# Optimization experiments

Measured on AMD Instinct MI355X. Metric: run time of the kernel, lower is better.

## Reference

```python
import jax, jax.numpy as jnp
import numpy as np

N_NODES = 100000


def _gcn_layer(x, W, b, src, dst, n):
    # PyG GCNConv: x' = D^-1/2 (A+I) D^-1/2 (x W) + b, with self-loops added.
    x = x @ W  # [N, out]
    loop = jnp.arange(n, dtype=src.dtype)
    src_f = jnp.concatenate([src, loop])
    dst_f = jnp.concatenate([dst, loop])
    deg = jax.ops.segment_sum(jnp.ones_like(dst_f, dtype=x.dtype), dst_f, num_segments=n)
    dinv = jnp.where(deg > 0, jax.lax.rsqrt(deg), 0.0)
    norm = dinv[src_f] * dinv[dst_f]  # [E+N]
    msgs = x[src_f] * norm[:, None]   # gather + scale
    out = jax.ops.segment_sum(msgs, dst_f, num_segments=n)
    return out + b


def setup_inputs() -> dict:
    key = jax.random.key(0)
    ks = jax.random.split(key, 16)
    inputFeatures = jax.random.normal(ks[0], (N_NODES, 64), dtype=jnp.float32)
    edge_index = jax.random.randint(ks[1], (2, 1000000), 0, N_NODES, dtype=jnp.int64)

    def lin(k, fan_in, fan_out):
        s = 1.0 / np.sqrt(fan_in)
        return jax.random.uniform(k, (fan_in, fan_out), jnp.float32, -s, s)

    return {
        "inputFeatures": inputFeatures,
        "W1": lin(ks[2], 64, 100), "b1": jnp.zeros((100,), jnp.float32),
        "W2": lin(ks[3], 100, 50), "b2": jnp.zeros((50,), jnp.float32),
        "W3": lin(ks[4], 50, 25), "b3": jnp.zeros((25,), jnp.float32),
        "Wl1": lin(ks[5], 25, 25), "bl1": jnp.zeros((25,), jnp.float32),
        "Wl2": lin(ks[6], 25, 10), "bl2": jnp.zeros((10,), jnp.float32),
        "Wl3": lin(ks[7], 10, 1), "bl3": jnp.zeros((1,), jnp.float32),
        "edge_index": edge_index,
    }


def reference(inputFeatures, W1, b1, W2, b2, W3, b3, Wl1, bl1, Wl2, bl2, Wl3, bl3, edge_index):
    src, dst = edge_index[0], edge_index[1]
    n = inputFeatures.shape[0]
    x = jax.nn.relu(_gcn_layer(inputFeatures, W1, b1, src, dst, n))
    x = jax.nn.relu(_gcn_layer(x, W2, b2, src, dst, n))
    x = jax.nn.relu(_gcn_layer(x, W3, b3, src, dst, n))
    x = jax.nn.relu(x @ Wl1 + bl1)
    x = jax.nn.relu(x @ Wl2 + bl2)
    x = jax.nn.relu(x @ Wl3 + bl3)
    return x  # [N, 1]
```

## Files before the change

kernel.cpp:

```cpp
#include <hip/hip_runtime.h>
#include <hip/hip_fp16.h>
#include <cstdint>

constexpr int BSHIFT = 9;
constexpr int NBUCK  = 256;
constexpr int BUCKET_CAP = 6144;
constexpr int BN = 1 << BSHIFT;

struct alignas(16) H8 { __half2 a, b, c, d; };
struct alignas(8)  H4 { __half2 a, b; };

typedef _Float16 f16x8 __attribute__((ext_vector_type(8)));
typedef float    f32x4 __attribute__((ext_vector_type(4)));

__device__ __forceinline__ float4 add4(float4 a, float4 b) {
    return make_float4(a.x + b.x, a.y + b.y, a.z + b.z, a.w + b.w);
}
__device__ __forceinline__ float4 mul4s(float4 a, float s) {
    return make_float4(a.x * s, a.y * s, a.z * s, a.w * s);
}
__device__ __forceinline__ void acc_h8(float4& A0, float4& A1, const H8 v, float s) {
    float2 f0 = __half22float2(v.a), f1 = __half22float2(v.b);
    float2 f2 = __half22float2(v.c), f3 = __half22float2(v.d);
    A0.x = fmaf(f0.x, s, A0.x); A0.y = fmaf(f0.y, s, A0.y);
    A0.z = fmaf(f1.x, s, A0.z); A0.w = fmaf(f1.y, s, A0.w);
    A1.x = fmaf(f2.x, s, A1.x); A1.y = fmaf(f2.y, s, A1.y);
    A1.z = fmaf(f3.x, s, A1.z); A1.w = fmaf(f3.y, s, A1.w);
}


constexpr int EPT = 16;
__global__ __launch_bounds__(256) void partition_pack(
    const int* __restrict__ src, const int* __restrict__ dst,
    int* __restrict__ bucketCur, int* __restrict__ pairs, int ne, int nEdgeBlocks,
    const float* __restrict__ W1, const float* __restrict__ W2,
    const float* __restrict__ W3,
    __half* __restrict__ P1, __half* __restrict__ P2, __half* __restrict__ P3) {
    if (blockIdx.x == (unsigned)nEdgeBlocks) {
        int t = threadIdx.x;
        for (int i = t; i < 7 * 2 * 64 * 8; i += 256) {
            int j = i & 7, lane = (i >> 3) & 63, f = i >> 9;
            int mt = f >> 1, kf = f & 1;
            int k = kf * 32 + (lane >> 4) * 8 + j;
            int m = mt * 16 + (lane & 15);
            P1[i] = __float2half_rn(m < 100 ? W1[k * 100 + m] : 0.0f);
        }
        for (int i = t; i < 4 * 4 * 64 * 8; i += 256) {
            int j = i & 7, lane = (i >> 3) & 63, f = i >> 9;
            int mt = f >> 2, kf = f & 3;
            int k = kf * 32 + (lane >> 4) * 8 + j;
            int m = mt * 16 + (lane & 15);
            P2[i] = __float2half_rn((k < 100 && m < 50) ? W2[k * 50 + m] : 0.0f);
        }
        for (int i = t; i < 2 * 2 * 64 * 8; i += 256) {
            int j = i & 7, lane = (i >> 3) & 63, f = i >> 9;
            int mt = f >> 1, kf = f & 1;
            int k = kf * 32 + (lane >> 4) * 8 + j;
            int m = mt * 16 + (lane & 15);
            P3[i] = __float2half_rn((k < 50 && m < 25) ? W3[k * 25 + m] : 0.0f);
        }
        return;
    }
    __shared__ int lcnt[NBUCK];
    __shared__ int lbase[NBUCK];
    int base = blockIdx.x * (256 * EPT);
    if (threadIdx.x < NBUCK) lcnt[threadIdx.x] = 0;
    __syncthreads();
    int2 ed[EPT];
    int  rnk[EPT];
#pragma unroll
    for (int j = 0; j < EPT; ++j) {
        int e = base + j * 256 + threadIdx.x;
        if (e < ne) {
            int d = dst[e];
            ed[j] = make_int2(src[e], d);
            rnk[j] = atomicAdd(&lcnt[d >> BSHIFT], 1);
        } else {
            ed[j].y = -1;
        }
    }
    __syncthreads();
    if (threadIdx.x < NBUCK) {
        int c = lcnt[threadIdx.x];
        lbase[threadIdx.x] = c ? atomicAdd(&bucketCur[threadIdx.x], c) : 0;
    }
    __syncthreads();
#pragma unroll
    for (int j = 0; j < EPT; ++j) {
        if (ed[j].y >= 0) {
            int b = ed[j].y >> BSHIFT;
            int p = lbase[b] + rnk[j];
            if (p < BUCKET_CAP)
                pairs[(size_t)b * BUCKET_CAP + p] =
                    (ed[j].x << BSHIFT) | (ed[j].y & (BN - 1));
        }
    }
}

__global__ __launch_bounds__(256) void bucket_csr_scan(
    const int* __restrict__ pairs, const int* __restrict__ bucketCnt,
    int* __restrict__ offs, float* __restrict__ dinv, int* __restrict__ csr,
    int n, int ne, int nbuckets) {
    __shared__ int hist[BN];
    __shared__ int cur[BN];
    __shared__ int tmp[256];
    __shared__ int baseS;
    int b = blockIdx.x;
    int t = threadIdx.x;

    int c = (t < (unsigned)nbuckets) ? bucketCnt[t] : 0;
    tmp[t] = c;
    __syncthreads();
    for (int off = 1; off < 256; off <<= 1) {
        int v = (t >= (unsigned)off) ? tmp[t - off] : 0;
        __syncthreads();
        tmp[t] += v;
        __syncthreads();
    }
    if (t == 0) {
        baseS = b ? tmp[b - 1] : 0;
        if (b == 0) offs[n] = ne;
    }
    __syncthreads();
    int base = baseS;
    int cnt  = bucketCnt[b];
    const int* pb = pairs + (size_t)b * BUCKET_CAP;
    int nodeLo = b << BSHIFT;

    hist[t] = 0;
    hist[t + 256] = 0;
    __syncthreads();
    for (int e = t; e < cnt; e += 256)
        atomicAdd(&hist[pb[e] & (BN - 1)], 1);
    __syncthreads();

    int l0 = 2 * t, l1 = l0 + 1;
    int h0 = hist[l0], h1 = hist[l1];
    tmp[t] = h0 + h1;
    __syncthreads();
    for (int off = 1; off < 256; off <<= 1) {
        int v = (t >= (unsigned)off) ? tmp[t - off] : 0;
        __syncthreads();
        tmp[t] += v;
        __syncthreads();
    }
    int e0 = tmp[t] - (h0 + h1);
    int e1 = e0 + h0;
    int g0 = nodeLo + l0, g1 = nodeLo + l1;
    if (g0 < n) { offs[g0] = base + e0; dinv[g0] = rsqrtf((float)(h0 + 1)); }
    if (g1 < n) { offs[g1] = base + e1; dinv[g1] = rsqrtf((float)(h1 + 1)); }
    cur[l0] = e0;
    cur[l1] = e1;
    __syncthreads();

    for (int e = t; e < cnt; e += 256) {
        int p = pb[e];
        int pos = atomicAdd(&cur[p & (BN - 1)], 1);
        csr[base + pos] = ((unsigned)p) >> BSHIFT;
    }
}

__global__ void cvt_scale_f32_f16(const float* __restrict__ x, const float* __restrict__ dinv,
                                  __half* __restrict__ o, int n4) {
    int i = blockIdx.x * blockDim.x + threadIdx.x;
    if (i < n4) {
        float dv = dinv[i >> 4];
        float4 v = ((const float4*)x)[i];
        H4 h;
        h.a = __floats2half2_rn(v.x * dv, v.y * dv);
        h.b = __floats2half2_rn(v.z * dv, v.w * dv);
        ((H4*)o)[i] = h;
    }
}

constexpr int XSP = 72;
constexpr int HPS = 136;
__global__ __launch_bounds__(256, 4) void agg1gemm12(
    const __half* __restrict__ x, const int* __restrict__ offs,
    const int* __restrict__ csr, const float* __restrict__ dinv,
    const __half* __restrict__ P1, const float* __restrict__ b1,
    const __half* __restrict__ P2, __half* __restrict__ out, int n) {
    __shared__ alignas(16) _Float16 Xs[64 * XSP];
    __shared__ alignas(16) _Float16 Hs[64 * HPS];
    int tid = threadIdx.x, lane = tid & 63, w = tid >> 6;
    int lg = lane >> 4, lr = lane & 15;
    int blockBase = blockIdx.x * 64;

    for (int i = tid; i < 64 * 2; i += 256) {
        f16x8 zz = {};
        *(f16x8*)&Hs[(i >> 1) * HPS + 112 + (i & 1) * 8] = zz;
    }

    int f0 = (lane & 7) * 8;
#pragma unroll
    for (int p = 0; p < 2; ++p) {
        int nl = w * 16 + p * 8 + (lane >> 3);
        int node = blockBase + nl;
        float4 z4 = make_float4(0.f, 0.f, 0.f, 0.f);
        float4 a00 = z4, a01 = z4, a10 = z4, a11 = z4, a20 = z4, a21 = z4, a30 = z4, a31 = z4;
        float dv = 0.0f;
        if (node < n) {
            dv = dinv[node];
            H8 sv = *(const H8*)&x[(size_t)node * 64 + f0];
            acc_h8(a00, a01, sv, 1.0f);
            int e0 = offs[node], e1 = offs[node + 1];
            int e = e0;
            for (; e + 4 <= e1; e += 4) {
                int i0 = csr[e], i1 = csr[e + 1], i2 = csr[e + 2], i3 = csr[e + 3];
                H8 v0 = *(const H8*)&x[(size_t)i0 * 64 + f0];
                H8 v1 = *(const H8*)&x[(size_t)i1 * 64 + f0];
                H8 v2 = *(const H8*)&x[(size_t)i2 * 64 + f0];
                H8 v3 = *(const H8*)&x[(size_t)i3 * 64 + f0];
                acc_h8(a00, a01, v0, 1.0f);
                acc_h8(a10, a11, v1, 1.0f);
                acc_h8(a20, a21, v2, 1.0f);
                acc_h8(a30, a31, v3, 1.0f);
            }
            for (; e < e1; ++e) {
                H8 v = *(const H8*)&x[(size_t)csr[e] * 64 + f0];
                acc_h8(a00, a01, v, 1.0f);
            }
        }
        float4 A0 = add4(add4(a00, a10), add4(a20, a30));
        float4 A1 = add4(add4(a01, a11), add4(a21, a31));
        A0 = mul4s(A0, dv);
        A1 = mul4s(A1, dv);
        H8 h;
        h.a = __floats2half2_rn(A0.x, A0.y);
        h.b = __floats2half2_rn(A0.z, A0.w);
        h.c = __floats2half2_rn(A1.x, A1.y);
        h.d = __floats2half2_rn(A1.z, A1.w);
        *(H8*)&Xs[nl * XSP + f0] = h;
    }
    __syncthreads();

    const f16x8* P1v = (const f16x8*)P1;
    float b1v[7];
#pragma unroll
    for (int mt = 0; mt < 7; ++mt) {
        int m = mt * 16 + lr;
        b1v[mt] = (m < 100) ? b1[m] : 0.0f;
    }
    {
        int rowL = w * 16 + lr;
        f16x8 a0 = *(const f16x8*)&Xs[rowL * XSP + lg * 8];
        f16x8 a1 = *(const f16x8*)&Xs[rowL * XSP + 32 + lg * 8];
        int hbase = w * 16;
#pragma unroll
        for (int mt = 0; mt < 7; ++mt) {
            f16x8 w0 = P1v[(mt * 2 + 0) * 64 + lane];
            f16x8 w1 = P1v[(mt * 2 + 1) * 64 + lane];
            f32x4 acc = {};
            acc = __builtin_amdgcn_mfma_f32_16x16x32_f16(a0, w0, acc, 0, 0, 0);
            acc = __builtin_amdgcn_mfma_f32_16x16x32_f16(a1, w1, acc, 0, 0, 0);
            int col = mt * 16 + lr;
#pragma unroll
            for (int i = 0; i < 4; ++i) {
                int rloc = hbase + lg * 4 + i;
                Hs[rloc * HPS + col] = (_Float16)fmaxf(acc[i] + b1v[mt], 0.0f);
            }
        }
    }
    __syncthreads();

    const f16x8* P2v = (const f16x8*)P2;
    int lbase = w * 16;
    const _Float16* hrow = &Hs[(size_t)(lbase + lr) * HPS];
    f16x8 a0 = *(const f16x8*)&hrow[lg * 8];
    f16x8 a1 = *(const f16x8*)&hrow[32 + lg * 8];
    f16x8 a2 = *(const f16x8*)&hrow[64 + lg * 8];
    f16x8 a3 = *(const f16x8*)&hrow[96 + lg * 8];
    float dvq[4];
#pragma unroll
    for (int i = 0; i < 4; ++i) {
        int node = blockBase + lbase + lg * 4 + i;
        dvq[i] = (node < n) ? dinv[node] : 0.0f;
    }
#pragma unroll
    for (int mt = 0; mt < 4; ++mt) {
        f16x8 w0 = P2v[(mt * 4 + 0) * 64 + lane];
        f16x8 w1 = P2v[(mt * 4 + 1) * 64 + lane];
        f16x8 w2 = P2v[(mt * 4 + 2) * 64 + lane];
        f16x8 w3 = P2v[(mt * 4 + 3) * 64 + lane];
        f32x4 acc = {};
        acc = __builtin_amdgcn_mfma_f32_16x16x32_f16(a0, w0, acc, 0, 0, 0);
        acc = __builtin_amdgcn_mfma_f32_16x16x32_f16(a1, w1, acc, 0, 0, 0);
        acc = __builtin_amdgcn_mfma_f32_16x16x32_f16(a2, w2, acc, 0, 0, 0);
        acc = __builtin_amdgcn_mfma_f32_16x16x32_f16(a3, w3, acc, 0, 0, 0);
        int col = mt * 16 + lr;
#pragma unroll
        for (int i = 0; i < 4; ++i)
            Xs[(lbase + lg * 4 + i) * XSP + col] = (_Float16)(acc[i] * dvq[i]);
    }
    __syncthreads();

    for (int i = tid; i < 64 * 8; i += 256) {
        int r = i >> 3, cc = (i & 7) * 8;
        int node = blockBase + r;
        if (node < n)
            *(H8*)&out[(size_t)node * 64 + cc] = *(const H8*)&Xs[r * XSP + cc];
    }
}

constexpr int YP = 72;
__global__ __launch_bounds__(256) void agg2g3(
    const __half* __restrict__ s, const int* __restrict__ offs,
    const int* __restrict__ csr, const float* __restrict__ dinv,
    const float* __restrict__ b2, const __half* __restrict__ P3,
    __half* __restrict__ out, int n) {
    __shared__ alignas(16) _Float16 Ys[32 * YP];
    int tid = threadIdx.x, lane = tid & 63, w = tid >> 6;
    int lg = lane >> 4, lr = lane & 15;
    int blockBase = blockIdx.x * 32;

    int nodeL = tid >> 3;
    int f0 = (tid & 7) * 8;
    int node = blockBase + nodeL;
    float v[8] = {0.f, 0.f, 0.f, 0.f, 0.f, 0.f, 0.f, 0.f};
    if (node < n && f0 < 56) {
        float dv = dinv[node];
        float4 z4 = make_float4(0.f, 0.f, 0.f, 0.f);
        float4 a00 = z4, a01 = z4, a10 = z4, a11 = z4, a20 = z4, a21 = z4, a30 = z4, a31 = z4;
        {
            H8 sv = *(const H8*)&s[(size_t)node * 64 + f0];
            acc_h8(a00, a01, sv, 1.0f);
        }
        int e0 = offs[node], e1 = offs[node + 1];
        int e = e0;
        for (; e + 4 <= e1; e += 4) {
            int i0 = csr[e], i1 = csr[e + 1], i2 = csr[e + 2], i3 = csr[e + 3];
            H8 v0 = *(const H8*)&s[(size_t)i0 * 64 + f0];
            H8 v1 = *(const H8*)&s[(size_t)i1 * 64 + f0];
            H8 v2 = *(const H8*)&s[(size_t)i2 * 64 + f0];
            H8 v3 = *(const H8*)&s[(size_t)i3 * 64 + f0];
            acc_h8(a00, a01, v0, 1.0f);
            acc_h8(a10, a11, v1, 1.0f);
            acc_h8(a20, a21, v2, 1.0f);
            acc_h8(a30, a31, v3, 1.0f);
        }
        for (; e < e1; ++e) {
            H8 vv = *(const H8*)&s[(size_t)csr[e] * 64 + f0];
            acc_h8(a00, a01, vv, 1.0f);
        }
        float4 A0 = add4(add4(a00, a10), add4(a20, a30));
        float4 A1 = add4(add4(a01, a11), add4(a21, a31));
        float vr[8] = {A0.x, A0.y, A0.z, A0.w, A1.x, A1.y, A1.z, A1.w};
#pragma unroll
        for (int i = 0; i < 8; ++i)
            v[i] = (f0 + i < 50) ? fmaxf(dv * vr[i] + b2[f0 + i], 0.0f) : 0.0f;
    }
    {
        H8 h;
        h.a = __floats2half2_rn(v[0], v[1]);
        h.b = __floats2half2_rn(v[2], v[3]);
        h.c = __floats2half2_rn(v[4], v[5]);
        h.d = __floats2half2_rn(v[6], v[7]);
        *(H8*)&Ys[nodeL * YP + f0] = h;
    }
    __syncthreads();

    int rt = w >> 1, mt = w & 1;
    const f16x8* P3v = (const f16x8*)P3;
    f16x8 w0 = P3v[(mt * 2 + 0) * 64 + lane];
    f16x8 w1 = P3v[(mt * 2 + 1) * 64 + lane];
    int rowL = rt * 16 + lr;
    f16x8 a0 = *(const f16x8*)&Ys[rowL * YP + lg * 8];
    f16x8 a1 = *(const f16x8*)&Ys[rowL * YP + 32 + lg * 8];
    f32x4 acc = {};
    acc = __builtin_amdgcn_mfma_f32_16x16x32_f16(a0, w0, acc, 0, 0, 0);
    acc = __builtin_amdgcn_mfma_f32_16x16x32_f16(a1, w1, acc, 0, 0, 0);
    __syncthreads();
    int col = mt * 16 + lr;
#pragma unroll
    for (int i = 0; i < 4; ++i) {
        int rl = rt * 16 + lg * 4 + i;
        int nd = blockBase + rl;
        float dv = (nd < n) ? dinv[nd] : 0.0f;
        Ys[rl * YP + col] = (_Float16)(acc[i] * dv);
    }
    __syncthreads();

    if (tid < 128) {
        int r = tid >> 2, cc = (tid & 3) * 8;
        int nd = blockBase + r;
        if (nd < n)
            *(H8*)&out[(size_t)nd * 32 + cc] = *(const H8*)&Ys[r * YP + cc];
    }
}

__global__ __launch_bounds__(256) void agg3_mlp_h(
    const __half* __restrict__ s, const int* __restrict__ offs,
    const int* __restrict__ csr, const float* __restrict__ dinv,
    const float* __restrict__ bg,
    const float* __restrict__ Wl1, const float* __restrict__ bl1,
    const float* __restrict__ Wl2, const float* __restrict__ bl2,
    const float* __restrict__ Wl3, const float* __restrict__ bl3,
    float* __restrict__ out, int n) {
    constexpr int LPN = 4;
    __shared__ float W1s[625], W2s[250], W3s[10], b1s[25], b2s[10];
    __shared__ float accs[64 * 26];
    __shared__ float b3s;

    for (int i = threadIdx.x; i < 625; i += 256) W1s[i] = Wl1[i];
    for (int i = threadIdx.x; i < 250; i += 256) W2s[i] = Wl2[i];
    if (threadIdx.x < 10) { W3s[threadIdx.x] = Wl3[threadIdx.x]; b2s[threadIdx.x] = bl2[threadIdx.x]; }
    if (threadIdx.x < 25) b1s[threadIdx.x] = bl1[threadIdx.x];
    if (threadIdx.x == 0) b3s = bl3[0];

    int lane = threadIdx.x % LPN;
    int nl   = threadIdx.x / LPN;
    int node = blockIdx.x * 64 + nl;
    int f0 = lane * 8;

    if (node < n && f0 < 25) {
        float dv = dinv[node];
        float4 z4 = make_float4(0.f, 0.f, 0.f, 0.f);
        float4 a00 = z4, a01 = z4, a10 = z4, a11 = z4, a20 = z4, a21 = z4, a30 = z4, a31 = z4;
        {
            H8 sv = *(const H8*)&s[(size_t)node * 32 + f0];
            acc_h8(a00, a01, sv, 1.0f);
        }
        int e0 = offs[node], e1 = offs[node + 1];
        int e = e0;
        for (; e + 4 <= e1; e += 4) {
            int i0 = csr[e], i1 = csr[e + 1], i2 = csr[e + 2], i3 = csr[e + 3];
            H8 v0 = *(const H8*)&s[(size_t)i0 * 32 + f0];
            H8 v1 = *(const H8*)&s[(size_t)i1 * 32 + f0];
            H8 v2 = *(const H8*)&s[(size_t)i2 * 32 + f0];
            H8 v3 = *(const H8*)&s[(size_t)i3 * 32 + f0];
            acc_h8(a00, a01, v0, 1.0f);
            acc_h8(a10, a11, v1, 1.0f);
            acc_h8(a20, a21, v2, 1.0f);
            acc_h8(a30, a31, v3, 1.0f);
        }
        for (; e < e1; ++e) {
            H8 v = *(const H8*)&s[(size_t)csr[e] * 32 + f0];
            acc_h8(a00, a01, v, 1.0f);
        }
        float4 A0 = add4(add4(a00, a10), add4(a20, a30));
        float4 A1 = add4(add4(a01, a11), add4(a21, a31));
        float v[8] = {A0.x, A0.y, A0.z, A0.w, A1.x, A1.y, A1.z, A1.w};
#pragma unroll
        for (int i = 0; i < 8; ++i)
            if (f0 + i < 25)
                accs[nl * 26 + f0 + i] = fmaxf(dv * v[i] + bg[f0 + i], 0.0f);
    }
    __syncthreads();

    if (threadIdx.x < 64) {
        int nd = blockIdx.x * 64 + threadIdx.x;
        if (nd < n) {
            const float* xr = &accs[threadIdx.x * 26];
            float h1[25];
#pragma unroll
            for (int m = 0; m < 25; ++m) {
                float a = b1s[m];
#pragma unroll
                for (int k = 0; k < 25; ++k) a = fmaf(xr[k], W1s[k * 25 + m], a);
                h1[m] = fmaxf(a, 0.0f);
            }
            float h2[10];
#pragma unroll
            for (int m = 0; m < 10; ++m) {
                float a = b2s[m];
#pragma unroll
                for (int k = 0; k < 25; ++k) a = fmaf(h1[k], W2s[k * 10 + m], a);
                h2[m] = fmaxf(a, 0.0f);
            }
            float a = b3s;
#pragma unroll
            for (int k = 0; k < 10; ++k) a = fmaf(h2[k], W3s[k], a);
            out[nd] = fmaxf(a, 0.0f);
        }
    }
}


extern "C" void kernel_launch(void* const* d_in, const int* in_sizes, int n_in,
                              void* d_out, int out_size, void* d_ws, size_t ws_size,
                              hipStream_t stream) {
    const float* x0  = (const float*)d_in[0];
    const float* W1  = (const float*)d_in[1];
    const float* b1  = (const float*)d_in[2];
    const float* W2  = (const float*)d_in[3];
    const float* b2  = (const float*)d_in[4];
    const float* W3  = (const float*)d_in[5];
    const float* b3  = (const float*)d_in[6];
    const float* Wl1 = (const float*)d_in[7];
    const float* bl1 = (const float*)d_in[8];
    const float* Wl2 = (const float*)d_in[9];
    const float* bl2 = (const float*)d_in[10];
    const float* Wl3 = (const float*)d_in[11];
    const float* bl3 = (const float*)d_in[12];
    const int*   edge = (const int*)d_in[13];

    int n  = in_sizes[0] / 64;
    int ne = in_sizes[13] / 2;
    const int* esrc = edge;
    const int* edst = edge + ne;

    char* ws = (char*)d_ws;
    auto alloc = [&](size_t bytes) {
        char* p = ws;
        ws += (bytes + 255) & ~(size_t)255;
        return p;
    };
    int*    offs       = (int*)alloc((size_t)(n + 1) * 4);
    int*    bucketCur  = (int*)alloc(NBUCK * 4);
    int*    csr        = (int*)alloc((size_t)ne * 4);
    float*  dinv       = (float*)alloc((size_t)n * 4);
    __half* x0h        = (__half*)alloc((size_t)n * 64 * 2);
    __half* bufDh      = (__half*)alloc((size_t)n * 64 * 2);
    __half* bufCh      = (__half*)alloc((size_t)n * 32 * 2);
    __half* P1         = (__half*)alloc(7 * 2 * 64 * 8 * 2);
    __half* P2         = (__half*)alloc(4 * 4 * 64 * 8 * 2);
    __half* P3         = (__half*)alloc(2 * 2 * 64 * 8 * 2);
    int*    pairs = (int*)bufDh;
    (void)ws_size; (void)n_in; (void)out_size;

    int nbuckets = (n + (1 << BSHIFT) - 1) >> BSHIFT;
    int nchunk   = (ne + 256 * EPT - 1) / (256 * EPT);

    hipMemsetAsync(bucketCur, 0, NBUCK * 4, stream);
    partition_pack<<<nchunk + 1, 256, 0, stream>>>(
        esrc, edst, bucketCur, pairs, ne, nchunk, W1, W2, W3, P1, P2, P3);
    bucket_csr_scan<<<nbuckets, 256, 0, stream>>>(
        pairs, bucketCur, offs, dinv, csr, n, ne, nbuckets);

    cvt_scale_f32_f16<<<(n * 16 + 255) / 256, 256, 0, stream>>>(x0, dinv, x0h, n * 16);

    agg1gemm12<<<(n + 63) / 64, 256, 0, stream>>>(
        x0h, offs, csr, dinv, P1, b1, P2, bufDh, n);

    agg2g3<<<(n + 31) / 32, 256, 0, stream>>>(
        bufDh, offs, csr, dinv, b2, P3, bufCh, n);

    agg3_mlp_h<<<(n + 63) / 64, 256, 0, stream>>>(
        bufCh, offs, csr, dinv, b3, Wl1, bl1, Wl2, bl2, Wl3, bl3, (float*)d_out, n);
}
```

Before: 228.3 us.

## Split 64-wide half feature buffers into two 32-wide planes for gather locality

Stores the layer-1 input and the layer-2 intermediate as two planar 32-column half arrays, not one 64-column array. The aggregation kernels now gather one plane at a time, so each pass works on a 64-byte row slice and a smaller working set that may sit better in cache. Each thread now handles 4 lanes per node, covering twice as many nodes per block, and loops over both planes. This re-walks the CSR edge list twice per node. agg2g3 also moves to 64-node blocks and computes both output tiles per wave.

New measurement: 242.2 us. 1.06x slower.

```diff
diff --git a/kernel.cpp b/kernel.cpp
--- a/kernel.cpp
+++ b/kernel.cpp
@@ -160,26 +160,30 @@
     }
 }
 
-__global__ void cvt_scale_f32_f16(const float* __restrict__ x, const float* __restrict__ dinv,
-                                  __half* __restrict__ o, int n4) {
+__global__ void cvt_scale_planar(const float* __restrict__ x, const float* __restrict__ dinv,
+                                 __half* __restrict__ oA, __half* __restrict__ oB, int n16) {
     int i = blockIdx.x * blockDim.x + threadIdx.x;
-    if (i < n4) {
-        float dv = dinv[i >> 4];
+    if (i < n16) {
+        int node = i >> 4, c = (i & 15) * 4;
+        float dv = dinv[node];
         float4 v = ((const float4*)x)[i];
         H4 h;
         h.a = __floats2half2_rn(v.x * dv, v.y * dv);
         h.b = __floats2half2_rn(v.z * dv, v.w * dv);
-        ((H4*)o)[i] = h;
+        if (c < 32) *(H4*)&oA[(size_t)node * 32 + c] = h;
+        else        *(H4*)&oB[(size_t)node * 32 + c - 32] = h;
     }
 }
 
 constexpr int XSP = 72;
 constexpr int HPS = 136;
 __global__ __launch_bounds__(256, 4) void agg1gemm12(
-    const __half* __restrict__ x, const int* __restrict__ offs,
-    const int* __restrict__ csr, const float* __restrict__ dinv,
+    const __half* __restrict__ xA, const __half* __restrict__ xB,
+    const int* __restrict__ offs, const int* __restrict__ csr,
+    const float* __restrict__ dinv,
     const __half* __restrict__ P1, const float* __restrict__ b1,
-    const __half* __restrict__ P2, __half* __restrict__ out, int n) {
+    const __half* __restrict__ P2,
+    __half* __restrict__ outA, __half* __restrict__ outB, int n) {
     __shared__ alignas(16) _Float16 Xs[64 * XSP];
     __shared__ alignas(16) _Float16 Hs[64 * HPS];
     int tid = threadIdx.x, lane = tid & 63, w = tid >> 6;
@@ -191,33 +195,34 @@
         *(f16x8*)&Hs[(i >> 1) * HPS + 112 + (i & 1) * 8] = zz;
     }
 
-    int f0 = (lane & 7) * 8;
-#pragma unroll
-    for (int p = 0; p < 2; ++p) {
-        int nl = w * 16 + p * 8 + (lane >> 3);
-        int node = blockBase + nl;
+    int nodeL = w * 16 + (lane >> 2);
+    int f0 = (lane & 3) * 8;
+    int node = blockBase + nodeL;
+#pragma unroll
+    for (int pl = 0; pl < 2; ++pl) {
+        const __half* xp = pl ? xB : xA;
         float4 z4 = make_float4(0.f, 0.f, 0.f, 0.f);
         float4 a00 = z4, a01 = z4, a10 = z4, a11 = z4, a20 = z4, a21 = z4, a30 = z4, a31 = z4;
         float dv = 0.0f;
         if (node < n) {
             dv = dinv[node];
-            H8 sv = *(const H8*)&x[(size_t)node * 64 + f0];
+            H8 sv = *(const H8*)&xp[(size_t)node * 32 + f0];
             acc_h8(a00, a01, sv, 1.0f);
             int e0 = offs[node], e1 = offs[node + 1];
             int e = e0;
             for (; e + 4 <= e1; e += 4) {
                 int i0 = csr[e], i1 = csr[e + 1], i2 = csr[e + 2], i3 = csr[e + 3];
-                H8 v0 = *(const H8*)&x[(size_t)i0 * 64 + f0];
-                H8 v1 = *(const H8*)&x[(size_t)i1 * 64 + f0];
-                H8 v2 = *(const H8*)&x[(size_t)i2 * 64 + f0];
-                H8 v3 = *(const H8*)&x[(size_t)i3 * 64 + f0];
+                H8 v0 = *(const H8*)&xp[(size_t)i0 * 32 + f0];
+                H8 v1 = *(const H8*)&xp[(size_t)i1 * 32 + f0];
+                H8 v2 = *(const H8*)&xp[(size_t)i2 * 32 + f0];
+                H8 v3 = *(const H8*)&xp[(size_t)i3 * 32 + f0];
                 acc_h8(a00, a01, v0, 1.0f);
                 acc_h8(a10, a11, v1, 1.0f);
                 acc_h8(a20, a21, v2, 1.0f);
                 acc_h8(a30, a31, v3, 1.0f);
             }
             for (; e < e1; ++e) {
-                H8 v = *(const H8*)&x[(size_t)csr[e] * 64 + f0];
+                H8 v = *(const H8*)&xp[(size_t)csr[e] * 32 + f0];
                 acc_h8(a00, a01, v, 1.0f);
             }
         }
@@ -230,7 +235,7 @@
         h.b = __floats2half2_rn(A0.z, A0.w);
         h.c = __floats2half2_rn(A1.x, A1.y);
         h.d = __floats2half2_rn(A1.z, A1.w);
-        *(H8*)&Xs[nl * XSP + f0] = h;
+        *(H8*)&Xs[nodeL * XSP + pl * 32 + f0] = h;
     }
     __syncthreads();
 
@@ -273,8 +278,8 @@
     float dvq[4];
 #pragma unroll
     for (int i = 0; i < 4; ++i) {
-        int node = blockBase + lbase + lg * 4 + i;
-        dvq[i] = (node < n) ? dinv[node] : 0.0f;
+        int nd = blockBase + lbase + lg * 4 + i;
+        dvq[i] = (nd < n) ? dinv[nd] : 0.0f;
     }
 #pragma unroll
     for (int mt = 0; mt < 4; ++mt) {
@@ -294,94 +299,101 @@
     }
     __syncthreads();
 
-    for (int i = tid; i < 64 * 8; i += 256) {
-        int r = i >> 3, cc = (i & 7) * 8;
-        int node = blockBase + r;
-        if (node < n)
-            *(H8*)&out[(size_t)node * 64 + cc] = *(const H8*)&Xs[r * XSP + cc];
+    for (int i = tid; i < 64 * 4; i += 256) {
+        int r = i >> 2, cc = (i & 3) * 8;
+        int nd = blockBase + r;
+        if (nd < n) {
+            *(H8*)&outA[(size_t)nd * 32 + cc] = *(const H8*)&Xs[r * XSP + cc];
+            *(H8*)&outB[(size_t)nd * 32 + cc] = *(const H8*)&Xs[r * XSP + 32 + cc];
+        }
     }
 }
 
 constexpr int YP = 72;
 __global__ __launch_bounds__(256) void agg2g3(
-    const __half* __restrict__ s, const int* __restrict__ offs,
-    const int* __restrict__ csr, const float* __restrict__ dinv,
+    const __half* __restrict__ sA, const __half* __restrict__ sB,
+    const int* __restrict__ offs, const int* __restrict__ csr,
+    const float* __restrict__ dinv,
     const float* __restrict__ b2, const __half* __restrict__ P3,
     __half* __restrict__ out, int n) {
-    __shared__ alignas(16) _Float16 Ys[32 * YP];
+    __shared__ alignas(16) _Float16 Ys[64 * YP];
     int tid = threadIdx.x, lane = tid & 63, w = tid >> 6;
     int lg = lane >> 4, lr = lane & 15;
-    int blockBase = blockIdx.x * 32;
-
-    int nodeL = tid >> 3;
-    int f0 = (tid & 7) * 8;
+    int blockBase = blockIdx.x * 64;
+
+    int nodeL = tid >> 2;
+    int f0 = (tid & 3) * 8;
     int node = blockBase + nodeL;
-    float v[8] = {0.f, 0.f, 0.f, 0.f, 0.f, 0.f, 0.f, 0.f};
-    if (node < n && f0 < 56) {
-        float dv = dinv[node];
-        float4 z4 = make_float4(0.f, 0.f, 0.f, 0.f);
-        float4 a00 = z4, a01 = z4, a10 = z4, a11 = z4, a20 = z4, a21 = z4, a30 = z4, a31 = z4;
-        {
-            H8 sv = *(const H8*)&s[(size_t)node * 64 + f0];
-            acc_h8(a00, a01, sv, 1.0f);
-        }
-        int e0 = offs[node], e1 = offs[node + 1];
-        int e = e0;
-        for (; e + 4 <= e1; e += 4) {
-            int i0 = csr[e], i1 = csr[e + 1], i2 = csr[e + 2], i3 = csr[e + 3];
-            H8 v0 = *(const H8*)&s[(size_t)i0 * 64 + f0];
-            H8 v1 = *(const H8*)&s[(size_t)i1 * 64 + f0];
-            H8 v2 = *(const H8*)&s[(size_t)i2 * 64 + f0];
-            H8 v3 = *(const H8*)&s[(size_t)i3 * 64 + f0];
-            acc_h8(a00, a01, v0, 1.0f);
-            acc_h8(a10, a11, v1, 1.0f);
-            acc_h8(a20, a21, v2, 1.0f);
-            acc_h8(a30, a31, v3, 1.0f);
-        }
-        for (; e < e1; ++e) {
-            H8 vv = *(const H8*)&s[(size_t)csr[e] * 64 + f0];
-            acc_h8(a00, a01, vv, 1.0f);
-        }
-        float4 A0 = add4(add4(a00, a10), add4(a20, a30));
-        float4 A1 = add4(add4(a01, a11), add4(a21, a31));
-        float vr[8] = {A0.x, A0.y, A0.z, A0.w, A1.x, A1.y, A1.z, A1.w};
-#pragma unroll
-        for (int i = 0; i < 8; ++i)
-            v[i] = (f0 + i < 50) ? fmaxf(dv * vr[i] + b2[f0 + i], 0.0f) : 0.0f;
-    }
-    {
+#pragma unroll
+    for (int pl = 0; pl < 2; ++pl) {
+        const __half* sp = pl ? sB : sA;
+        int cbase = pl * 32;
+        float v[8] = {0.f, 0.f, 0.f, 0.f, 0.f, 0.f, 0.f, 0.f};
+        if (node < n) {
+            float dv = dinv[node];
+            float4 z4 = make_float4(0.f, 0.f, 0.f, 0.f);
+            float4 a00 = z4, a01 = z4, a10 = z4, a11 = z4, a20 = z4, a21 = z4, a30 = z4, a31 = z4;
+            {
+                H8 sv = *(const H8*)&sp[(size_t)node * 32 + f0];
+                acc_h8(a00, a01, sv, 1.0f);
+            }
+            int e0 = offs[node], e1 = offs[node + 1];
+            int e = e0;
+            for (; e + 4 <= e1; e += 4) {
+                int i0 = csr[e], i1 = csr[e + 1], i2 = csr[e + 2], i3 = csr[e + 3];
+                H8 v0 = *(const H8*)&sp[(size_t)i0 * 32 + f0];
+                H8 v1 = *(const H8*)&sp[(size_t)i1 * 32 + f0];
+                H8 v2 = *(const H8*)&sp[(size_t)i2 * 32 + f0];
+                H8 v3 = *(const H8*)&sp[(size_t)i3 * 32 + f0];
+                acc_h8(a00, a01, v0, 1.0f);
+                acc_h8(a10, a11, v1, 1.0f);
+                acc_h8(a20, a21, v2, 1.0f);
+                acc_h8(a30, a31, v3, 1.0f);
+            }
+            for (; e < e1; ++e) {
+                H8 vv = *(const H8*)&sp[(size_t)csr[e] * 32 + f0];
+                acc_h8(a00, a01, vv, 1.0f);
+            }
+            float4 A0 = add4(add4(a00, a10), add4(a20, a30));
+            float4 A1 = add4(add4(a01, a11), add4(a21, a31));
+            float vr[8] = {A0.x, A0.y, A0.z, A0.w, A1.x, A1.y, A1.z, A1.w};
+#pragma unroll
+            for (int i = 0; i < 8; ++i) {
+                int col = cbase + f0 + i;
+                v[i] = (col < 50) ? fmaxf(dv * vr[i] + b2[col], 0.0f) : 0.0f;
+            }
+        }
         H8 h;
         h.a = __floats2half2_rn(v[0], v[1]);
         h.b = __floats2half2_rn(v[2], v[3]);
         h.c = __floats2half2_rn(v[4], v[5]);
         h.d = __floats2half2_rn(v[6], v[7]);
-        *(H8*)&Ys[nodeL * YP + f0] = h;
-    }
-    __syncthreads();
-
-    int rt = w >> 1, mt = w & 1;
+        *(H8*)&Ys[nodeL * YP + cbase + f0] = h;
+    }
+    __syncthreads();
+
     const f16x8* P3v = (const f16x8*)P3;
-    f16x8 w0 = P3v[(mt * 2 + 0) * 64 + lane];
-    f16x8 w1 = P3v[(mt * 2 + 1) * 64 + lane];
-    int rowL = rt * 16 + lr;
+    int rowL = w * 16 + lr;
     f16x8 a0 = *(const f16x8*)&Ys[rowL * YP + lg * 8];
     f16x8 a1 = *(const f16x8*)&Ys[rowL * YP + 32 + lg * 8];
-    f32x4 acc = {};
-    acc = __builtin_amdgcn_mfma_f32_16x16x32_f16(a0, w0, acc, 0, 0, 0);
-    acc = __builtin_amdgcn_mfma_f32_16x16x32_f16(a1, w1, acc, 0, 0, 0);
-    __syncthreads();
-    int col = mt * 16 + lr;
+    f32x4 acc0 = {}, acc1 = {};
+    acc0 = __builtin_amdgcn_mfma_f32_16x16x32_f16(a0, P3v[0 * 64 + lane], acc0, 0, 0, 0);
+    acc0 = __builtin_amdgcn_mfma_f32_16x16x32_f16(a1, P3v[1 * 64 + lane], acc0, 0, 0, 0);
+    acc1 = __builtin_amdgcn_mfma_f32_16x16x32_f16(a0, P3v[2 * 64 + lane], acc1, 0, 0, 0);
+    acc1 = __builtin_amdgcn_mfma_f32_16x16x32_f16(a1, P3v[3 * 64 + lane], acc1, 0, 0, 0);
+    __syncthreads();
 #pragma unroll
     for (int i = 0; i < 4; ++i) {
-        int rl = rt * 16 + lg * 4 + i;
+        int rl = w * 16 + lg * 4 + i;
         int nd = blockBase + rl;
         float dv = (nd < n) ? dinv[nd] : 0.0f;
-        Ys[rl * YP + col] = (_Float16)(acc[i] * dv);
-    }
-    __syncthreads();
-
-    if (tid < 128) {
-        int r = tid >> 2, cc = (tid & 3) * 8;
+        Ys[rl * YP + lr]      = (_Float16)(acc0[i] * dv);
+        Ys[rl * YP + 16 + lr] = (_Float16)(acc1[i] * dv);
+    }
+    __syncthreads();
+
+    for (int i = tid; i < 64 * 4; i += 256) {
+        int r = i >> 2, cc = (i & 3) * 8;
         int nd = blockBase + r;
         if (nd < n)
             *(H8*)&out[(size_t)nd * 32 + cc] = *(const H8*)&Ys[r * YP + cc];
@@ -509,13 +521,15 @@
     int*    bucketCur  = (int*)alloc(NBUCK * 4);
     int*    csr        = (int*)alloc((size_t)ne * 4);
     float*  dinv       = (float*)alloc((size_t)n * 4);
-    __half* x0h        = (__half*)alloc((size_t)n * 64 * 2);
-    __half* bufDh      = (__half*)alloc((size_t)n * 64 * 2);
+    __half* x0hA       = (__half*)alloc((size_t)n * 32 * 2);
+    __half* x0hB       = (__half*)alloc((size_t)n * 32 * 2);
+    __half* bufDhA     = (__half*)alloc((size_t)n * 32 * 2);
+    __half* bufDhB     = (__half*)alloc((size_t)n * 32 * 2);
     __half* bufCh      = (__half*)alloc((size_t)n * 32 * 2);
     __half* P1         = (__half*)alloc(7 * 2 * 64 * 8 * 2);
     __half* P2         = (__half*)alloc(4 * 4 * 64 * 8 * 2);
     __half* P3         = (__half*)alloc(2 * 2 * 64 * 8 * 2);
-    int*    pairs = (int*)bufDh;
+    int*    pairs = (int*)bufDhA;
     (void)ws_size; (void)n_in; (void)out_size;
 
     int nbuckets = (n + (1 << BSHIFT) - 1) >> BSHIFT;
@@ -527,13 +541,13 @@
     bucket_csr_scan<<<nbuckets, 256, 0, stream>>>(
         pairs, bucketCur, offs, dinv, csr, n, ne, nbuckets);
 
-    cvt_scale_f32_f16<<<(n * 16 + 255) / 256, 256, 0, stream>>>(x0, dinv, x0h, n * 16);
+    cvt_scale_planar<<<(n * 16 + 255) / 256, 256, 0, stream>>>(x0, dinv, x0hA, x0hB, n * 16);
 
     agg1gemm12<<<(n + 63) / 64, 256, 0, stream>>>(
-        x0h, offs, csr, dinv, P1, b1, P2, bufDh, n);
-
-    agg2g3<<<(n + 31) / 32, 256, 0, stream>>>(
-        bufDh, offs, csr, dinv, b2, P3, bufCh, n);
+        x0hA, x0hB, offs, csr, dinv, P1, b1, P2, bufDhA, bufDhB, n);
+
+    agg2g3<<<(n + 63) / 64, 256, 0, stream>>>(
+        bufDhA, bufDhB, offs, csr, dinv, b2, P3, bufCh, n);
 
     agg3_mlp_h<<<(n + 63) / 64, 256, 0, stream>>>(
         bufCh, offs, csr, dinv, b3, Wl1, bl1, Wl2, bl2, Wl3, bl3, (float*)d_out, n);
```
